# Performance work log

Measured on AMD Instinct MI355X. Metric: run time of the kernel, lower is better.

Reference implementation:

```python
import jax, jax.numpy as jnp
import numpy as np

C = 256  # hidden_channels
N = 262144  # number of nodes


def setup_inputs() -> dict:
    key = jax.random.key(0)
    ks = jax.random.split(key, 6)
    s = 1.0 / np.sqrt(C)
    return {
        "x": jax.random.normal(ks[0], (N, C), dtype=jnp.float32),
        "Wq": jax.random.uniform(ks[1], (C, C), jnp.float32, -s, s),
        "Wk": jax.random.uniform(ks[2], (C, C), jnp.float32, -s, s),
        "Wv": jax.random.uniform(ks[3], (C, C), jnp.float32, -s, s),
        "Wo": jax.random.uniform(ks[4], (C, C), jnp.float32, -s, s),
        "bo": jax.random.uniform(ks[5], (C,), jnp.float32, -s, s),
    }


def reference(x, Wq, Wk, Wv, Wo, bo):
    # torch nn.Linear: y = x @ W.T
    q = jax.nn.elu(x @ Wq.T) + 1.0          # [N, C], strictly positive feature map
    k = jax.nn.elu(x @ Wk.T) + 1.0          # [N, C]
    v = x @ Wv.T                             # [N, C]
    kv = k.T @ v                             # [C, C] aggregate
    z = 1.0 / jnp.maximum(q @ k.sum(axis=0), 1e-6)  # [N] normalizer
    h = (q @ kv) * z[:, None]                # [N, C]
    # dropout p=0.0 (and eval mode) -> identity
    return h @ Wo.T + bo
```

## Files before the change

kernel.cpp:

```cpp
#include <hip/hip_runtime.h>
#include <cstdint>


typedef __attribute__((ext_vector_type(8))) short short8;
typedef __attribute__((ext_vector_type(4))) float f32x4;
typedef unsigned short u16;
typedef unsigned int u32;

#define MFMA16(a, b, c) __builtin_amdgcn_mfma_f32_16x16x32_bf16(a, b, c, 0, 0, 0)

__device__ __forceinline__ u32 bf16_1(float f) {
  u32 u = __float_as_uint(f);
  return (u + 0x7FFFu + ((u >> 16) & 1u)) >> 16;
}
__device__ __forceinline__ u32 bf16pk(float lo, float hi) {
  return bf16_1(lo) | (bf16_1(hi) << 16);
}

__global__ void prep_kernel(const float* __restrict__ Wq, const float* __restrict__ Wk,
                            const float* __restrict__ Wv, u16* __restrict__ WqF,
                            u16* __restrict__ WkF, u16* __restrict__ WvF,
                            float* __restrict__ kvp, float* __restrict__ ksum,
                            int E, int S) {
  int id = blockIdx.x * 256 + threadIdx.x;
  if (id < 256) ksum[id] = 0.f;
  for (int t = id; t < 3 * 65536; t += 65536) {
    int mat = t >> 16;
    int e = t & 65535;
    int c = e >> 8, d = e & 255;
    const float* src = (mat == 0) ? Wq : (mat == 1) ? Wk : Wv;
    u16* dst = (mat == 0) ? WqF : (mat == 1) ? WkF : WvF;
    int idx = (((c >> 5) * 8 + (d >> 5)) * 2 + ((c >> 4) & 1)) * 512 +
              ((d >> 3) & 3) * 128 + (c & 15) * 8 + (d & 7);
    dst[idx] = (u16)bf16_1(src[e]);
  }
  if (S > 0) {
    float4 z4 = {0.f, 0.f, 0.f, 0.f};
    float4* kz = (float4*)(kvp + (size_t)E * 65536);
    int total = S * 16384;
    for (int t = id; t < total; t += 65536) kz[t] = z4;
  }
}

__global__ __launch_bounds__(1024, 4) void phase1_kernel(
    const float* __restrict__ x, const u16* __restrict__ WkF,
    const u16* __restrict__ WvF, float* __restrict__ kvp, float* __restrict__ ksum,
    int E, int S) {
  __shared__ __align__(16) u16 xv_l[16384];
  __shared__ __align__(16) u16 kT_l[16384];
  const int tid = threadIdx.x;
  const int lane = tid & 63;
  const int w = tid >> 6;
  const int m = lane & 15;
  const int q = lane >> 4;
  const int wg = blockIdx.x;

  const f32x4 fz = {0.f, 0.f, 0.f, 0.f};
  f32x4 kvacc[16];
#pragma unroll
  for (int tr = 0; tr < 16; ++tr) kvacc[tr] = fz;
  float ksl = 0.f;

  const int fb0 = (((w >> 1) * 8) * 2 + (w & 1)) * 512 + lane * 8;
  const int sdb = (tid & 63) >> 1;
  const int ssw = sdb & 7;
  const int scw = 4 * (tid & 1);
  const int srb = tid >> 6;
  const int col = 16 * w + m;

  for (int it = 0; it < 16; ++it) {
    const int row0 = wg * 1024 + it * 64;
    __syncthreads();
    {
      const float4* xp = (const float4*)(x + (size_t)row0 * 256);
      float4 f0 = xp[tid];
      float4 f1 = xp[1024 + tid];
      float4 f2 = xp[2048 + tid];
      float4 f3 = xp[3072 + tid];
      uint2 u;
      u.x = bf16pk(f0.x, f0.y); u.y = bf16pk(f0.z, f0.w);
      *(uint2*)&xv_l[sdb * 512 + (((srb) ^ ssw) << 3) + scw] = u;
      u.x = bf16pk(f1.x, f1.y); u.y = bf16pk(f1.z, f1.w);
      *(uint2*)&xv_l[sdb * 512 + (((16 + srb) ^ ssw) << 3) + scw] = u;
      u.x = bf16pk(f2.x, f2.y); u.y = bf16pk(f2.z, f2.w);
      *(uint2*)&xv_l[sdb * 512 + (((32 + srb) ^ ssw) << 3) + scw] = u;
      u.x = bf16pk(f3.x, f3.y); u.y = bf16pk(f3.z, f3.w);
      *(uint2*)&xv_l[sdb * 512 + (((48 + srb) ^ ssw) << 3) + scw] = u;
    }
    __syncthreads();
    f32x4 kacc[4], vacc[4];
#pragma unroll
    for (int rt = 0; rt < 4; ++rt) { kacc[rt] = fz; vacc[rt] = fz; }
#pragma unroll
    for (int ks = 0; ks < 8; ++ks) {
      const int fb = fb0 + ks * 1024;
      short8 wk = *(const short8*)(WkF + fb);
      short8 wv = *(const short8*)(WvF + fb);
      const int db = 4 * ks + q;
      const int sw = db & 7;
      const u16* xb = &xv_l[db * 512];
#pragma unroll
      for (int rt = 0; rt < 4; ++rt) {
        short8 af = *(const short8*)&xb[((16 * rt + m) ^ sw) << 3];
        kacc[rt] = MFMA16(af, wk, kacc[rt]);
        vacc[rt] = MFMA16(af, wv, vacc[rt]);
      }
    }
    __syncthreads();
#pragma unroll
    for (int rt = 0; rt < 4; ++rt) {
      f32x4 kk = kacc[rt];
      float e0 = kk[0] > 0.f ? kk[0] + 1.f : __expf(kk[0]);
      float e1 = kk[1] > 0.f ? kk[1] + 1.f : __expf(kk[1]);
      float e2 = kk[2] > 0.f ? kk[2] + 1.f : __expf(kk[2]);
      float e3 = kk[3] > 0.f ? kk[3] + 1.f : __expf(kk[3]);
      ksl += (e0 + e1) + (e2 + e3);
      int pos = (2 * rt + (q >> 1)) * 2048 + col * 8 + 4 * (q & 1);
      uint2 kp;
      kp.x = bf16pk(e0, e1);
      kp.y = bf16pk(e2, e3);
      *(uint2*)&kT_l[pos] = kp;
      f32x4 vv = vacc[rt];
      uint2 vp;
      vp.x = bf16pk(vv[0], vv[1]);
      vp.y = bf16pk(vv[2], vv[3]);
      *(uint2*)&xv_l[pos] = vp;
    }
    __syncthreads();
#pragma unroll
    for (int kc = 0; kc < 2; ++kc) {
      const int rbb = (4 * kc + q) * 2048;
      short8 bf = *(const short8*)&xv_l[rbb + col * 8];
#pragma unroll
      for (int tr = 0; tr < 16; ++tr) {
        short8 af = *(const short8*)&kT_l[rbb + (16 * tr + m) * 8];
        kvacc[tr] = MFMA16(af, bf, kvacc[tr]);
      }
    }
  }
  float s = ksl;
  s += __shfl_xor(s, 16);
  s += __shfl_xor(s, 32);
  if (q == 0) atomicAdd(&ksum[col], s);
  const int slot = (wg < E) ? wg : (E + ((wg - E) & (S - 1)));
  float* dst = kvp + (size_t)slot * 65536;
  if (wg < E) {
#pragma unroll
    for (int tr = 0; tr < 16; ++tr)
#pragma unroll
      for (int e = 0; e < 4; ++e)
        dst[(16 * tr + 4 * q + e) * 256 + col] = kvacc[tr][e];
  } else {
#pragma unroll
    for (int tr = 0; tr < 16; ++tr)
#pragma unroll
      for (int e = 0; e < 4; ++e)
        atomicAdd(&dst[(16 * tr + 4 * q + e) * 256 + col], kvacc[tr][e]);
  }
}

__global__ void mid1_kernel(const float* __restrict__ kvp, float* __restrict__ kv_red,
                            int nslots) {
  int id = blockIdx.x * 256 + threadIdx.x;
  float4 s = {0.f, 0.f, 0.f, 0.f};
  const float4* kp = (const float4*)kvp;
  for (int p = 0; p < nslots; ++p) {
    float4 v = kp[(size_t)p * 16384 + id];
    s.x += v.x; s.y += v.y; s.z += v.z; s.w += v.w;
  }
  ((float4*)kv_red)[id] = s;
}

__global__ void mid2_kernel(const float* __restrict__ kv_red,
                            const float* __restrict__ Wo, u16* __restrict__ MF) {
  __shared__ float kr[256];
  const int i = blockIdx.x;
  const int j = threadIdx.x;
  kr[j] = kv_red[i * 256 + j];
  __syncthreads();
  float acc = 0.f;
  const float* wo = Wo + (size_t)j * 256;
#pragma unroll 8
  for (int c = 0; c < 256; ++c) acc += kr[c] * wo[c];
  MF[(((j >> 5) * 8 + (i >> 5)) * 2 + ((j >> 4) & 1)) * 512 + ((i >> 3) & 3) * 128 +
     (j & 15) * 8 + (i & 7)] = (u16)bf16_1(acc);
}

__global__ __launch_bounds__(1024, 4) void phase2_kernel(
    const float* __restrict__ x, const u16* __restrict__ WqF,
    const u16* __restrict__ MF, const float* __restrict__ ksum,
    const float* __restrict__ bo, float* __restrict__ out) {
  __shared__ __align__(16) u16 xq_l[16384];
  __shared__ float s_l[64];
  const int tid = threadIdx.x;
  const int lane = tid & 63;
  const int w = tid >> 6;
  const int m = lane & 15;
  const int q = lane >> 4;
  const int wg = blockIdx.x;
  const f32x4 fz = {0.f, 0.f, 0.f, 0.f};

  const int fb0 = (((w >> 1) * 8) * 2 + (w & 1)) * 512 + lane * 8;
  short8 mf[8];
#pragma unroll
  for (int ks = 0; ks < 8; ++ks) mf[ks] = *(const short8*)(MF + fb0 + ks * 1024);
  const float ks0 = ksum[16 * w + m];
  const float b0 = bo[16 * w + m];

  const int sdb = (tid & 63) >> 1;
  const int ssw = sdb & 7;
  const int scw = 4 * (tid & 1);
  const int srb = tid >> 6;
  const int cq = 16 * w + m;

  float4 pf0, pf1, pf2, pf3;
  {
    const float4* xp = (const float4*)(x + (size_t)wg * 1024 * 256);
    pf0 = xp[tid]; pf1 = xp[1024 + tid]; pf2 = xp[2048 + tid]; pf3 = xp[3072 + tid];
  }

  for (int it = 0; it < 16; ++it) {
    const int row0 = wg * 1024 + it * 64;
    __syncthreads();
    {
      uint2 u;
      u.x = bf16pk(pf0.x, pf0.y); u.y = bf16pk(pf0.z, pf0.w);
      *(uint2*)&xq_l[sdb * 512 + (((srb) ^ ssw) << 3) + scw] = u;
      u.x = bf16pk(pf1.x, pf1.y); u.y = bf16pk(pf1.z, pf1.w);
      *(uint2*)&xq_l[sdb * 512 + (((16 + srb) ^ ssw) << 3) + scw] = u;
      u.x = bf16pk(pf2.x, pf2.y); u.y = bf16pk(pf2.z, pf2.w);
      *(uint2*)&xq_l[sdb * 512 + (((32 + srb) ^ ssw) << 3) + scw] = u;
      u.x = bf16pk(pf3.x, pf3.y); u.y = bf16pk(pf3.z, pf3.w);
      *(uint2*)&xq_l[sdb * 512 + (((48 + srb) ^ ssw) << 3) + scw] = u;
      if (tid < 64) s_l[tid] = 0.f;
    }
    __syncthreads();
    if (it < 15) {
      const float4* xp = (const float4*)(x + (size_t)(row0 + 64) * 256);
      pf0 = xp[tid]; pf1 = xp[1024 + tid]; pf2 = xp[2048 + tid]; pf3 = xp[3072 + tid];
    }
    f32x4 qacc[4];
#pragma unroll
    for (int rt = 0; rt < 4; ++rt) qacc[rt] = fz;
#pragma unroll
    for (int ks = 0; ks < 8; ++ks) {
      short8 wq = *(const short8*)(WqF + fb0 + ks * 1024);
      const int db = 4 * ks + q;
      const int sw = db & 7;
      const u16* xb = &xq_l[db * 512];
#pragma unroll
      for (int rt = 0; rt < 4; ++rt) {
        short8 af = *(const short8*)&xb[((16 * rt + m) ^ sw) << 3];
        qacc[rt] = MFMA16(af, wq, qacc[rt]);
      }
    }
#pragma unroll
    for (int rt = 0; rt < 4; ++rt) {
      f32x4 a = qacc[rt];
      a[0] = a[0] > 0.f ? a[0] + 1.f : __expf(a[0]);
      a[1] = a[1] > 0.f ? a[1] + 1.f : __expf(a[1]);
      a[2] = a[2] > 0.f ? a[2] + 1.f : __expf(a[2]);
      a[3] = a[3] > 0.f ? a[3] + 1.f : __expf(a[3]);
      qacc[rt] = a;
#pragma unroll
      for (int e = 0; e < 4; ++e) {
        float val = a[e] * ks0;
        val += __shfl_xor(val, 1);
        val += __shfl_xor(val, 2);
        val += __shfl_xor(val, 4);
        val += __shfl_xor(val, 8);
        if (m == 0) atomicAdd(&s_l[16 * rt + 4 * q + e], val);
      }
    }
    __syncthreads();
    {
      const int dbq = cq >> 3, swq = dbq & 7, cwq = cq & 7;
#pragma unroll
      for (int rt = 0; rt < 4; ++rt)
#pragma unroll
        for (int e = 0; e < 4; ++e) {
          int r = 16 * rt + 4 * q + e;
          xq_l[dbq * 512 + ((r ^ swq) << 3) + cwq] = (u16)bf16_1(qacc[rt][e]);
        }
    }
    __syncthreads();
    f32x4 tacc[4];
#pragma unroll
    for (int rt = 0; rt < 4; ++rt) tacc[rt] = fz;
#pragma unroll
    for (int ks = 0; ks < 8; ++ks) {
      const int db = 4 * ks + q;
      const int sw = db & 7;
      const u16* xb = &xq_l[db * 512];
#pragma unroll
      for (int rt = 0; rt < 4; ++rt) {
        short8 af = *(const short8*)&xb[((16 * rt + m) ^ sw) << 3];
        tacc[rt] = MFMA16(af, mf[ks], tacc[rt]);
      }
    }
#pragma unroll
    for (int rt = 0; rt < 4; ++rt)
#pragma unroll
      for (int e = 0; e < 4; ++e) {
        int r = 16 * rt + 4 * q + e;
        float z = __builtin_amdgcn_rcpf(fmaxf(s_l[r], 1e-6f));
        out[(size_t)(row0 + r) * 256 + cq] = tacc[rt][e] * z + b0;
      }
  }
}

extern "C" void kernel_launch(void* const* d_in, const int* in_sizes, int n_in,
                              void* d_out, int out_size, void* d_ws, size_t ws_size,
                              hipStream_t stream) {
  const float* x = (const float*)d_in[0];
  const float* Wq = (const float*)d_in[1];
  const float* Wk = (const float*)d_in[2];
  const float* Wv = (const float*)d_in[3];
  const float* Wo = (const float*)d_in[4];
  const float* bo = (const float*)d_in[5];
  float* out = (float*)d_out;

  const size_t fixedB = 1024 + 262144 + 4 * 131072;
  long long avail = (long long)ws_size - (long long)fixedB;
  int slots = avail > 0 ? (int)(avail / 262144) : 1;
  if (slots < 1) slots = 1;
  if (slots > 256) slots = 256;
  int E, S;
  if (slots >= 256) { E = 256; S = 0; }
  else if (slots >= 8) { E = slots - 4; S = 4; }
  else if (slots >= 2) { E = slots - 1; S = 1; }
  else { E = 0; S = 1; }
  const int nslots = E + S;

  char* base = (char*)d_ws;
  float* kvp = (float*)base;
  float* ksum = (float*)(base + (size_t)nslots * 262144);
  float* kvred = ksum + 256;
  u16* MF = (u16*)(kvred + 65536);
  u16* WqF = MF + 65536;
  u16* WkF = WqF + 65536;
  u16* WvF = WkF + 65536;

  prep_kernel<<<256, 256, 0, stream>>>(Wq, Wk, Wv, WqF, WkF, WvF, kvp, ksum, E, S);
  phase1_kernel<<<256, 1024, 0, stream>>>(x, WkF, WvF, kvp, ksum, E, S);
  mid1_kernel<<<64, 256, 0, stream>>>(kvp, kvred, nslots);
  mid2_kernel<<<256, 256, 0, stream>>>(kvred, Wo, MF);
  phase2_kernel<<<256, 1024, 0, stream>>>(x, WqF, MF, ksum, bo, out);
}
```

Measured before the change: 1.047 ms.

## Double-buffer x staging in both phases, fuse slot reduction, vectorize output stores

Both phase kernels now double-buffer the bf16 x tile in LDS. The next tile is staged while the kv-outer-product or the output GEMM runs, which removes one barrier per iteration. Phase 1 gets a separate vT buffer. The partial-kv slot reduction is folded into mid2, which drops a kernel launch and an intermediate buffer. Phase 2 swaps the MFMA operand order so each lane writes four contiguous outputs as a float4 nontemporal store, with a double-buffered normalizer. In exchange, LDS use per block goes up, which may limit occupancy.

```diff
diff --git a/kernel.cpp b/kernel.cpp
--- a/kernel.cpp
+++ b/kernel.cpp
@@ -46,8 +46,9 @@
     const float* __restrict__ x, const u16* __restrict__ WkF,
     const u16* __restrict__ WvF, float* __restrict__ kvp, float* __restrict__ ksum,
     int E, int S) {
-  __shared__ __align__(16) u16 xv_l[16384];
+  __shared__ __align__(16) u16 xb_l[2][16384];
   __shared__ __align__(16) u16 kT_l[16384];
+  __shared__ __align__(16) u16 vT_l[16384];
   const int tid = threadIdx.x;
   const int lane = tid & 63;
   const int w = tid >> 6;
@@ -64,30 +65,29 @@
   const int fb0 = (((w >> 1) * 8) * 2 + (w & 1)) * 512 + lane * 8;
   const int sdb = (tid & 63) >> 1;
   const int ssw = sdb & 7;
-  const int scw = 4 * (tid & 1);
+  const int spos0 = sdb * 512 + 4 * (tid & 1);
   const int srb = tid >> 6;
   const int col = 16 * w + m;
 
+  auto stage = [&](u16* dst, const float4* xp) {
+    float4 f0 = xp[tid], f1 = xp[1024 + tid];
+    uint2 u;
+    u.x = bf16pk(f0.x, f0.y); u.y = bf16pk(f0.z, f0.w);
+    *(uint2*)&dst[spos0 + ((srb ^ ssw) << 3)] = u;
+    u.x = bf16pk(f1.x, f1.y); u.y = bf16pk(f1.z, f1.w);
+    *(uint2*)&dst[spos0 + (((16 + srb) ^ ssw) << 3)] = u;
+    float4 f2 = xp[2048 + tid], f3 = xp[3072 + tid];
+    u.x = bf16pk(f2.x, f2.y); u.y = bf16pk(f2.z, f2.w);
+    *(uint2*)&dst[spos0 + (((32 + srb) ^ ssw) << 3)] = u;
+    u.x = bf16pk(f3.x, f3.y); u.y = bf16pk(f3.z, f3.w);
+    *(uint2*)&dst[spos0 + (((48 + srb) ^ ssw) << 3)] = u;
+  };
+
+  stage(xb_l[0], (const float4*)(x + (size_t)wg * 1024 * 256));
+  __syncthreads();
+
   for (int it = 0; it < 16; ++it) {
-    const int row0 = wg * 1024 + it * 64;
-    __syncthreads();
-    {
-      const float4* xp = (const float4*)(x + (size_t)row0 * 256);
-      float4 f0 = xp[tid];
-      float4 f1 = xp[1024 + tid];
-      float4 f2 = xp[2048 + tid];
-      float4 f3 = xp[3072 + tid];
-      uint2 u;
-      u.x = bf16pk(f0.x, f0.y); u.y = bf16pk(f0.z, f0.w);
-      *(uint2*)&xv_l[sdb * 512 + (((srb) ^ ssw) << 3) + scw] = u;
-      u.x = bf16pk(f1.x, f1.y); u.y = bf16pk(f1.z, f1.w);
-      *(uint2*)&xv_l[sdb * 512 + (((16 + srb) ^ ssw) << 3) + scw] = u;
-      u.x = bf16pk(f2.x, f2.y); u.y = bf16pk(f2.z, f2.w);
-      *(uint2*)&xv_l[sdb * 512 + (((32 + srb) ^ ssw) << 3) + scw] = u;
-      u.x = bf16pk(f3.x, f3.y); u.y = bf16pk(f3.z, f3.w);
-      *(uint2*)&xv_l[sdb * 512 + (((48 + srb) ^ ssw) << 3) + scw] = u;
-    }
-    __syncthreads();
+    const u16* xcur = xb_l[it & 1];
     f32x4 kacc[4], vacc[4];
 #pragma unroll
     for (int rt = 0; rt < 4; ++rt) { kacc[rt] = fz; vacc[rt] = fz; }
@@ -98,15 +98,14 @@
       short8 wv = *(const short8*)(WvF + fb);
       const int db = 4 * ks + q;
       const int sw = db & 7;
-      const u16* xb = &xv_l[db * 512];
+      const u16* xbp = &xcur[db * 512];
 #pragma unroll
       for (int rt = 0; rt < 4; ++rt) {
-        short8 af = *(const short8*)&xb[((16 * rt + m) ^ sw) << 3];
+        short8 af = *(const short8*)&xbp[((16 * rt + m) ^ sw) << 3];
         kacc[rt] = MFMA16(af, wk, kacc[rt]);
         vacc[rt] = MFMA16(af, wv, vacc[rt]);
       }
     }
-    __syncthreads();
 #pragma unroll
     for (int rt = 0; rt < 4; ++rt) {
       f32x4 kk = kacc[rt];
@@ -124,19 +123,23 @@
       uint2 vp;
       vp.x = bf16pk(vv[0], vv[1]);
       vp.y = bf16pk(vv[2], vv[3]);
-      *(uint2*)&xv_l[pos] = vp;
+      *(uint2*)&vT_l[pos] = vp;
     }
     __syncthreads();
+    if (it < 15)
+      stage(xb_l[(it + 1) & 1],
+            (const float4*)(x + (size_t)(wg * 1024 + (it + 1) * 64) * 256));
 #pragma unroll
     for (int kc = 0; kc < 2; ++kc) {
       const int rbb = (4 * kc + q) * 2048;
-      short8 bf = *(const short8*)&xv_l[rbb + col * 8];
+      short8 bf = *(const short8*)&vT_l[rbb + col * 8];
 #pragma unroll
       for (int tr = 0; tr < 16; ++tr) {
         short8 af = *(const short8*)&kT_l[rbb + (16 * tr + m) * 8];
         kvacc[tr] = MFMA16(af, bf, kvacc[tr]);
       }
     }
+    __syncthreads();
   }
   float s = ksl;
   s += __shfl_xor(s, 16);
@@ -159,39 +162,33 @@
   }
 }
 
-__global__ void mid1_kernel(const float* __restrict__ kvp, float* __restrict__ kv_red,
+__global__ void mid2_kernel(const float* __restrict__ kvp,
+                            const float* __restrict__ Wo, u16* __restrict__ MFt,
                             int nslots) {
-  int id = blockIdx.x * 256 + threadIdx.x;
-  float4 s = {0.f, 0.f, 0.f, 0.f};
-  const float4* kp = (const float4*)kvp;
-  for (int p = 0; p < nslots; ++p) {
-    float4 v = kp[(size_t)p * 16384 + id];
-    s.x += v.x; s.y += v.y; s.z += v.z; s.w += v.w;
-  }
-  ((float4*)kv_red)[id] = s;
-}
-
-__global__ void mid2_kernel(const float* __restrict__ kv_red,
-                            const float* __restrict__ Wo, u16* __restrict__ MF) {
   __shared__ float kr[256];
   const int i = blockIdx.x;
   const int j = threadIdx.x;
-  kr[j] = kv_red[i * 256 + j];
+  float s = 0.f;
+  const float* src = kvp + i * 256 + j;
+#pragma unroll 4
+  for (int p = 0; p < nslots; ++p) s += src[(size_t)p * 65536];
+  kr[j] = s;
   __syncthreads();
   float acc = 0.f;
   const float* wo = Wo + (size_t)j * 256;
 #pragma unroll 8
   for (int c = 0; c < 256; ++c) acc += kr[c] * wo[c];
-  MF[(((j >> 5) * 8 + (i >> 5)) * 2 + ((j >> 4) & 1)) * 512 + ((i >> 3) & 3) * 128 +
-     (j & 15) * 8 + (i & 7)] = (u16)bf16_1(acc);
+  MFt[((j >> 4) * 8 + (i >> 5)) * 512 + (((i >> 3) & 3) * 16 + (j & 15)) * 8 +
+      (i & 7)] = (u16)bf16_1(acc);
 }
 
 __global__ __launch_bounds__(1024, 4) void phase2_kernel(
     const float* __restrict__ x, const u16* __restrict__ WqF,
-    const u16* __restrict__ MF, const float* __restrict__ ksum,
+    const u16* __restrict__ MFt, const float* __restrict__ ksum,
     const float* __restrict__ bo, float* __restrict__ out) {
-  __shared__ __align__(16) u16 xq_l[16384];
-  __shared__ float s_l[64];
+  __shared__ __align__(16) u16 xb_l[2][16384];
+  __shared__ __align__(16) u16 qb_l[16384];
+  __shared__ float s_l[2][64];
   const int tid = threadIdx.x;
   const int lane = tid & 63;
   const int w = tid >> 6;
@@ -201,44 +198,43 @@
   const f32x4 fz = {0.f, 0.f, 0.f, 0.f};
 
   const int fb0 = (((w >> 1) * 8) * 2 + (w & 1)) * 512 + lane * 8;
-  short8 mf[8];
-#pragma unroll
-  for (int ks = 0; ks < 8; ++ks) mf[ks] = *(const short8*)(MF + fb0 + ks * 1024);
+  short8 mft[8];
+#pragma unroll
+  for (int ks = 0; ks < 8; ++ks)
+    mft[ks] = *(const short8*)(MFt + (w * 8 + ks) * 512 + lane * 8);
   const float ks0 = ksum[16 * w + m];
-  const float b0 = bo[16 * w + m];
+  const float4 bvec = *(const float4*)(bo + 16 * w + 4 * q);
 
   const int sdb = (tid & 63) >> 1;
   const int ssw = sdb & 7;
-  const int scw = 4 * (tid & 1);
+  const int spos0 = sdb * 512 + 4 * (tid & 1);
   const int srb = tid >> 6;
-  const int cq = 16 * w + m;
-
-  float4 pf0, pf1, pf2, pf3;
-  {
-    const float4* xp = (const float4*)(x + (size_t)wg * 1024 * 256);
-    pf0 = xp[tid]; pf1 = xp[1024 + tid]; pf2 = xp[2048 + tid]; pf3 = xp[3072 + tid];
-  }
+  const int dbq = (16 * w + m) >> 3;
+  const int swq = dbq & 7;
+  const int cwq = m & 7;
+
+  auto stage = [&](u16* dst, const float4* xp) {
+    float4 f0 = xp[tid], f1 = xp[1024 + tid];
+    uint2 u;
+    u.x = bf16pk(f0.x, f0.y); u.y = bf16pk(f0.z, f0.w);
+    *(uint2*)&dst[spos0 + ((srb ^ ssw) << 3)] = u;
+    u.x = bf16pk(f1.x, f1.y); u.y = bf16pk(f1.z, f1.w);
+    *(uint2*)&dst[spos0 + (((16 + srb) ^ ssw) << 3)] = u;
+    float4 f2 = xp[2048 + tid], f3 = xp[3072 + tid];
+    u.x = bf16pk(f2.x, f2.y); u.y = bf16pk(f2.z, f2.w);
+    *(uint2*)&dst[spos0 + (((32 + srb) ^ ssw) << 3)] = u;
+    u.x = bf16pk(f3.x, f3.y); u.y = bf16pk(f3.z, f3.w);
+    *(uint2*)&dst[spos0 + (((48 + srb) ^ ssw) << 3)] = u;
+  };
+
+  stage(xb_l[0], (const float4*)(x + (size_t)wg * 1024 * 256));
+  if (tid < 64) s_l[0][tid] = 0.f;
+  __syncthreads();
 
   for (int it = 0; it < 16; ++it) {
+    const u16* xcur = xb_l[it & 1];
+    const int sp = it & 1;
     const int row0 = wg * 1024 + it * 64;
-    __syncthreads();
-    {
-      uint2 u;
-      u.x = bf16pk(pf0.x, pf0.y); u.y = bf16pk(pf0.z, pf0.w);
-      *(uint2*)&xq_l[sdb * 512 + (((srb) ^ ssw) << 3) + scw] = u;
-      u.x = bf16pk(pf1.x, pf1.y); u.y = bf16pk(pf1.z, pf1.w);
-      *(uint2*)&xq_l[sdb * 512 + (((16 + srb) ^ ssw) << 3) + scw] = u;
-      u.x = bf16pk(pf2.x, pf2.y); u.y = bf16pk(pf2.z, pf2.w);
-      *(uint2*)&xq_l[sdb * 512 + (((32 + srb) ^ ssw) << 3) + scw] = u;
-      u.x = bf16pk(pf3.x, pf3.y); u.y = bf16pk(pf3.z, pf3.w);
-      *(uint2*)&xq_l[sdb * 512 + (((48 + srb) ^ ssw) << 3) + scw] = u;
-      if (tid < 64) s_l[tid] = 0.f;
-    }
-    __syncthreads();
-    if (it < 15) {
-      const float4* xp = (const float4*)(x + (size_t)(row0 + 64) * 256);
-      pf0 = xp[tid]; pf1 = xp[1024 + tid]; pf2 = xp[2048 + tid]; pf3 = xp[3072 + tid];
-    }
     f32x4 qacc[4];
 #pragma unroll
     for (int rt = 0; rt < 4; ++rt) qacc[rt] = fz;
@@ -247,10 +243,10 @@
       short8 wq = *(const short8*)(WqF + fb0 + ks * 1024);
       const int db = 4 * ks + q;
       const int sw = db & 7;
-      const u16* xb = &xq_l[db * 512];
+      const u16* xbp = &xcur[db * 512];
 #pragma unroll
       for (int rt = 0; rt < 4; ++rt) {
-        short8 af = *(const short8*)&xb[((16 * rt + m) ^ sw) << 3];
+        short8 af = *(const short8*)&xbp[((16 * rt + m) ^ sw) << 3];
         qacc[rt] = MFMA16(af, wq, qacc[rt]);
       }
     }
@@ -261,7 +257,6 @@
       a[1] = a[1] > 0.f ? a[1] + 1.f : __expf(a[1]);
       a[2] = a[2] > 0.f ? a[2] + 1.f : __expf(a[2]);
       a[3] = a[3] > 0.f ? a[3] + 1.f : __expf(a[3]);
-      qacc[rt] = a;
 #pragma unroll
       for (int e = 0; e < 4; ++e) {
         float val = a[e] * ks0;
@@ -269,21 +264,19 @@
         val += __shfl_xor(val, 2);
         val += __shfl_xor(val, 4);
         val += __shfl_xor(val, 8);
-        if (m == 0) atomicAdd(&s_l[16 * rt + 4 * q + e], val);
+        if (m == 0) atomicAdd(&s_l[sp][16 * rt + 4 * q + e], val);
+      }
+#pragma unroll
+      for (int e = 0; e < 4; ++e) {
+        int r = 16 * rt + 4 * q + e;
+        qb_l[dbq * 512 + ((r ^ swq) << 3) + cwq] = (u16)bf16_1(a[e]);
       }
     }
     __syncthreads();
-    {
-      const int dbq = cq >> 3, swq = dbq & 7, cwq = cq & 7;
-#pragma unroll
-      for (int rt = 0; rt < 4; ++rt)
-#pragma unroll
-        for (int e = 0; e < 4; ++e) {
-          int r = 16 * rt + 4 * q + e;
-          xq_l[dbq * 512 + ((r ^ swq) << 3) + cwq] = (u16)bf16_1(qacc[rt][e]);
-        }
-    }
-    __syncthreads();
+    if (it < 15)
+      stage(xb_l[(it + 1) & 1],
+            (const float4*)(x + (size_t)(row0 + 64) * 256));
+    if (tid < 64) s_l[sp ^ 1][tid] = 0.f;
     f32x4 tacc[4];
 #pragma unroll
     for (int rt = 0; rt < 4; ++rt) tacc[rt] = fz;
@@ -291,21 +284,25 @@
     for (int ks = 0; ks < 8; ++ks) {
       const int db = 4 * ks + q;
       const int sw = db & 7;
-      const u16* xb = &xq_l[db * 512];
+      const u16* xq = &qb_l[db * 512];
 #pragma unroll
       for (int rt = 0; rt < 4; ++rt) {
-        short8 af = *(const short8*)&xb[((16 * rt + m) ^ sw) << 3];
-        tacc[rt] = MFMA16(af, mf[ks], tacc[rt]);
-      }
-    }
-#pragma unroll
-    for (int rt = 0; rt < 4; ++rt)
-#pragma unroll
-      for (int e = 0; e < 4; ++e) {
-        int r = 16 * rt + 4 * q + e;
-        float z = __builtin_amdgcn_rcpf(fmaxf(s_l[r], 1e-6f));
-        out[(size_t)(row0 + r) * 256 + cq] = tacc[rt][e] * z + b0;
-      }
+        short8 af = *(const short8*)&xq[((16 * rt + m) ^ sw) << 3];
+        tacc[rt] = MFMA16(mft[ks], af, tacc[rt]);
+      }
+    }
+#pragma unroll
+    for (int rt = 0; rt < 4; ++rt) {
+      float zz = __builtin_amdgcn_rcpf(fmaxf(s_l[sp][16 * rt + m], 1e-6f));
+      f32x4 o;
+      o[0] = tacc[rt][0] * zz + bvec.x;
+      o[1] = tacc[rt][1] * zz + bvec.y;
+      o[2] = tacc[rt][2] * zz + bvec.z;
+      o[3] = tacc[rt][3] * zz + bvec.w;
+      f32x4* op = (f32x4*)(out + (size_t)(row0 + 16 * rt + m) * 256 + 16 * w + 4 * q);
+      __builtin_nontemporal_store(o, op);
+    }
+    __syncthreads();
   }
 }
 
@@ -320,7 +317,7 @@
   const float* bo = (const float*)d_in[5];
   float* out = (float*)d_out;
 
-  const size_t fixedB = 1024 + 262144 + 4 * 131072;
+  const size_t fixedB = 1024 + 4 * 131072;
   long long avail = (long long)ws_size - (long long)fixedB;
   int slots = avail > 0 ? (int)(avail / 262144) : 1;
   if (slots < 1) slots = 1;
@@ -335,15 +332,13 @@
   char* base = (char*)d_ws;
   float* kvp = (float*)base;
   float* ksum = (float*)(base + (size_t)nslots * 262144);
-  float* kvred = ksum + 256;
-  u16* MF = (u16*)(kvred + 65536);
-  u16* WqF = MF + 65536;
+  u16* MFt = (u16*)(ksum + 256);
+  u16* WqF = MFt + 65536;
   u16* WkF = WqF + 65536;
   u16* WvF = WkF + 65536;
 
   prep_kernel<<<256, 256, 0, stream>>>(Wq, Wk, Wv, WqF, WkF, WvF, kvp, ksum, E, S);
   phase1_kernel<<<256, 1024, 0, stream>>>(x, WkF, WvF, kvp, ksum, E, S);
-  mid1_kernel<<<64, 256, 0, stream>>>(kvp, kvred, nslots);
-  mid2_kernel<<<256, 256, 0, stream>>>(kvred, Wo, MF);
-  phase2_kernel<<<256, 1024, 0, stream>>>(x, WqF, MF, ksum, bo, out);
-}
+  mid2_kernel<<<256, 256, 0, stream>>>(kvp, Wo, MFt, nslots);
+  phase2_kernel<<<256, 1024, 0, stream>>>(x, WqF, MFt, ksum, bo, out);
+}
```

After: 1.016 ms. 2.9% less time.
